# Kernel tuning notes

Measured on AMD Instinct MI355X. Metric: run time of the kernel, lower is better.

The kernel has to match this reference:

```python
import jax, jax.numpy as jnp
import numpy as np

N_NODES = 10000
N_EDGES = 640000
HIDDEN = 128
OUT = 10

def setup_inputs() -> dict:
    key = jax.random.key(0)
    k1, k2, k3, k4 = jax.random.split(key, 4)
    x = jax.random.normal(k1, (N_NODES, HIDDEN), dtype=jnp.float32)
    edge_index = jax.random.randint(k2, (2, N_EDGES), 0, N_NODES, dtype=jnp.int64)
    # ClassifierMLP2 params: Linear(2*hidden -> hidden) -> ReLU -> Linear(hidden -> out)
    W1 = jax.random.normal(k3, (2 * HIDDEN, HIDDEN), dtype=jnp.float32) / np.sqrt(2 * HIDDEN)
    b1 = jnp.zeros((HIDDEN,), dtype=jnp.float32)
    W2 = jax.random.normal(k4, (HIDDEN, OUT), dtype=jnp.float32) / np.sqrt(HIDDEN)
    b2 = jnp.zeros((OUT,), dtype=jnp.float32)
    return {"x": x, "edge_index": edge_index, "W1": W1, "b1": b1, "W2": W2, "b2": b2}

def reference(x, edge_index, W1, b1, W2, b2):
    # mix_node_features(..., node_feat_mixing='cat'): gather src/dst node
    # embeddings per edge and concatenate along feature dim -> [E, 2*H]
    src, dst = edge_index[0], edge_index[1]
    edges_x = jnp.concatenate([x[src], x[dst]], axis=-1)  # [E, 2H]
    # ClassifierMLP2 (dropout inactive at inference)
    h = jax.nn.relu(edges_x @ W1 + b1)                    # [E, H]
    return h @ W2 + b2                                    # [E, OUT]
```

## Files before the change

kernel.cpp:

```cpp
#include <hip/hip_runtime.h>


typedef _Float16 f16;
typedef _Float16 f16x8 __attribute__((ext_vector_type(8)));
typedef float    f32x4 __attribute__((ext_vector_type(4)));

#define HID  128
#define TWOH 256
#define OUTD 10

__global__ __launch_bounds__(256) void prep_weights(
    const float* __restrict__ W1,
    const float* __restrict__ W2,
    f16* __restrict__ W1P,
    f16* __restrict__ W2P)
{
    const int slot = blockIdx.x * 256 + threadIdx.x;
    if (slot < 4096) {
        const int lane = slot & 63, i = slot >> 6;
        const int r = lane & 15, g = lane >> 4;
        const int wv = i >> 4, ct = (i >> 2) & 3, st = i & 3;
        const int c = wv * 64 + ct * 16 + r;
        f16x8 v;
#pragma unroll
        for (int j = 0; j < 8; ++j) {
            const int k = st * 32 + g * 8 + j;
            const float w = (c < HID) ? W1[k * HID + c]
                                      : W1[(HID + k) * HID + (c - HID)];
            v[j] = (f16)w;
        }
        *(f16x8*)(W1P + (long)slot * 8) = v;
    } else if (slot < 4096 + 256) {
        const int s2 = slot - 4096;
        const int lane = s2 & 63, st = s2 >> 6;
        const int r = lane & 15, g = lane >> 4;
        f16x8 v;
#pragma unroll
        for (int j = 0; j < 8; ++j)
            v[j] = (r < OUTD) ? (f16)W2[(st * 32 + g * 8 + j) * OUTD + r] : (f16)0.f;
        *(f16x8*)(W2P + (long)s2 * 8) = v;
    }
}

__global__ __launch_bounds__(256, 3) void node_AB(
    const float* __restrict__ x,
    const f16* __restrict__ W1P,
    const float* __restrict__ b1,
    f16* __restrict__ AB,
    int n_nodes)
{
    const int t = threadIdx.x;
    const int lane = t & 63;
    const int r = lane & 15, g = lane >> 4;
    const int wv = t >> 6;
    const int n0 = blockIdx.x * 16;

    const int xrow = (n0 + r < n_nodes) ? (n0 + r) : (n_nodes - 1);
    float4 xl[4][2];
#pragma unroll
    for (int st = 0; st < 4; ++st) {
        const float* xp = x + (long)xrow * HID + st * 32 + g * 8;
        xl[st][0] = *(const float4*)xp;
        xl[st][1] = *(const float4*)(xp + 4);
    }

    f16x8 w1f[4][4];
    float bias[4];
#pragma unroll
    for (int ct = 0; ct < 4; ++ct) {
        const int c = wv * 64 + ct * 16 + r;
        bias[ct] = (c < HID) ? b1[c] : 0.f;
#pragma unroll
        for (int st = 0; st < 4; ++st)
            w1f[ct][st] = *(const f16x8*)(W1P + ((long)((wv * 16 + ct * 4 + st)) * 64 + lane) * 8);
    }

    f32x4 acc[4] = {{0,0,0,0},{0,0,0,0},{0,0,0,0},{0,0,0,0}};
#pragma unroll
    for (int st = 0; st < 4; ++st) {
        f16x8 a;
        a[0] = (f16)xl[st][0].x; a[1] = (f16)xl[st][0].y;
        a[2] = (f16)xl[st][0].z; a[3] = (f16)xl[st][0].w;
        a[4] = (f16)xl[st][1].x; a[5] = (f16)xl[st][1].y;
        a[6] = (f16)xl[st][1].z; a[7] = (f16)xl[st][1].w;
#pragma unroll
        for (int ct = 0; ct < 4; ++ct)
            acc[ct] = __builtin_amdgcn_mfma_f32_16x16x32_f16(a, w1f[ct][st], acc[ct], 0, 0, 0);
    }

#pragma unroll
    for (int ct = 0; ct < 4; ++ct) {
        const int c = wv * 64 + ct * 16 + r;
#pragma unroll
        for (int q = 0; q < 4; ++q) {
            const int node = n0 + g * 4 + q;
            if (node < n_nodes)
                AB[(long)node * TWOH + c] = (f16)(acc[ct][q] + bias[ct]);
        }
    }
}

__global__ __launch_bounds__(256, 3) void edge_mlp(
    const f16* __restrict__ AB,
    const int* __restrict__ ei,
    const f16* __restrict__ W2P,
    const float* __restrict__ b2,
    float* __restrict__ out,
    int n_edges)
{
    const int t = threadIdx.x;
    const int lane = t & 63;
    const int r = lane & 15, g = lane >> 4;
    const int wv = t >> 6;

    f16x8 w2f[4];
#pragma unroll
    for (int st = 0; st < 4; ++st)
        w2f[st] = *(const f16x8*)(W2P + ((long)st * 64 + lane) * 8);
    const int rc = (r < OUTD) ? r : 0;
    const float bj = b2[rc];

    const f16x8* __restrict__ ABv = (const f16x8*)AB;
    const long eb = (long)blockIdx.x * 512 + wv * 128;

    int sn[8], dn[8];
#pragma unroll
    for (int it = 0; it < 8; ++it) {
        const long e = eb + it * 16 + r;
        const long ec = (e < n_edges) ? e : (n_edges - 1);
        sn[it] = ei[ec];
        dn[it] = ei[(long)n_edges + ec];
    }

    const f16x8 zt = {0, 0, 0, 0, 0, 0, 0, 0};

#define GATHER(Pa, Pc, IT)                                                  \
    f16x8 Pa[4], Pc[4];                                                     \
    {                                                                       \
        const long ab_ = (long)sn[IT] * 32, bb_ = (long)dn[IT] * 32;        \
        _Pragma("unroll")                                                   \
        for (int st = 0; st < 4; ++st) {                                    \
            Pa[st] = ABv[ab_ + st * 4 + g];                                 \
            Pc[st] = ABv[bb_ + 16 + st * 4 + g];                            \
        }                                                                   \
    }

#define COMPSTORE(Pa, Pc, IT)                                               \
    {                                                                       \
        f32x4 acc = {0, 0, 0, 0};                                           \
        _Pragma("unroll")                                                   \
        for (int st = 0; st < 4; ++st) {                                    \
            const f16x8 s = __builtin_elementwise_max(Pa[st] + Pc[st], zt); \
            acc = __builtin_amdgcn_mfma_f32_16x16x32_f16(s, w2f[st], acc, 0, 0, 0); \
        }                                                                   \
        if (r < OUTD) {                                                     \
            _Pragma("unroll")                                               \
            for (int q = 0; q < 4; ++q) {                                   \
                const long ee = eb + IT * 16 + g * 4 + q;                   \
                if (ee < n_edges) out[ee * OUTD + r] = acc[q] + bj;         \
            }                                                               \
        }                                                                   \
    }

    GATHER(a0, c0, 0)
    GATHER(a1, c1, 1)
    GATHER(a2, c2, 2)
    __builtin_amdgcn_sched_barrier(0);
    COMPSTORE(a0, c0, 0)
    GATHER(a3, c3, 3)
    __builtin_amdgcn_sched_barrier(0);
    COMPSTORE(a1, c1, 1)
    GATHER(a4, c4, 4)
    __builtin_amdgcn_sched_barrier(0);
    COMPSTORE(a2, c2, 2)
    GATHER(a5, c5, 5)
    __builtin_amdgcn_sched_barrier(0);
    COMPSTORE(a3, c3, 3)
    GATHER(a6, c6, 6)
    __builtin_amdgcn_sched_barrier(0);
    COMPSTORE(a4, c4, 4)
    GATHER(a7, c7, 7)
    __builtin_amdgcn_sched_barrier(0);
    COMPSTORE(a5, c5, 5)
    COMPSTORE(a6, c6, 6)
    COMPSTORE(a7, c7, 7)

#undef GATHER
#undef COMPSTORE
}

extern "C" void kernel_launch(void* const* d_in, const int* in_sizes, int n_in,
                              void* d_out, int out_size, void* d_ws, size_t ws_size,
                              hipStream_t stream) {
    const float* x  = (const float*)d_in[0];
    const int*   ei = (const int*)d_in[1];
    const float* W1 = (const float*)d_in[2];
    const float* b1 = (const float*)d_in[3];
    const float* W2 = (const float*)d_in[4];
    const float* b2 = (const float*)d_in[5];
    float* out = (float*)d_out;

    const int n_nodes = in_sizes[0] / HID;
    const int n_edges = in_sizes[1] / 2;

    f16* AB  = (f16*)d_ws;
    f16* W1P = AB + (long)n_nodes * TWOH;
    f16* W2P = W1P + 4096 * 8;

    prep_weights<<<17, 256, 0, stream>>>(W1, W2, W1P, W2P);

    node_AB<<<(n_nodes + 15) / 16, 256, 0, stream>>>(x, W1P, b1, AB, n_nodes);

    edge_mlp<<<(n_edges + 511) / 512, 256, 0, stream>>>(AB, ei, W2P, b2, out, n_edges);
}
```

Measured before the change: 61.78 us.

## Hand-schedule edge gathers with inline asm loads and LDS-staged coalesced stores

Replaces compiler-generated gathers in edge_mlp with inline-asm global_load_dwordx4 using immediate offsets, and explicit s_waitcnt vmcnt counts to keep three edge tiles of loads in flight. Output for each 16-edge tile is staged through shared memory so 40 lanes write contiguous dwordx4 stores instead of scattered scalar stores. A scalar fallback path handles partial tiles. This adds asm fragility: the waitcnt counts must match the vector memory ops actually issued, including the interleaved stores.

Measured after the change: 60.35 us. 1.02x faster.

```diff
diff --git a/kernel.cpp b/kernel.cpp
--- a/kernel.cpp
+++ b/kernel.cpp
@@ -108,6 +108,7 @@
     float* __restrict__ out,
     int n_edges)
 {
+    __shared__ float stage[4][160];
     const int t = threadIdx.x;
     const int lane = t & 63;
     const int r = lane & 15, g = lane >> 4;
@@ -117,10 +118,8 @@
 #pragma unroll
     for (int st = 0; st < 4; ++st)
         w2f[st] = *(const f16x8*)(W2P + ((long)st * 64 + lane) * 8);
-    const int rc = (r < OUTD) ? r : 0;
-    const float bj = b2[rc];
-
-    const f16x8* __restrict__ ABv = (const f16x8*)AB;
+    const float bj = b2[(r < OUTD) ? r : 0];
+
     const long eb = (long)blockIdx.x * 512 + wv * 128;
 
     int sn[8], dn[8];
@@ -134,59 +133,96 @@
 
     const f16x8 zt = {0, 0, 0, 0, 0, 0, 0, 0};
 
-#define GATHER(Pa, Pc, IT)                                                  \
-    f16x8 Pa[4], Pc[4];                                                     \
-    {                                                                       \
-        const long ab_ = (long)sn[IT] * 32, bb_ = (long)dn[IT] * 32;        \
-        _Pragma("unroll")                                                   \
-        for (int st = 0; st < 4; ++st) {                                    \
-            Pa[st] = ABv[ab_ + st * 4 + g];                                 \
-            Pc[st] = ABv[bb_ + 16 + st * 4 + g];                            \
-        }                                                                   \
-    }
-
-#define COMPSTORE(Pa, Pc, IT)                                               \
-    {                                                                       \
-        f32x4 acc = {0, 0, 0, 0};                                           \
-        _Pragma("unroll")                                                   \
-        for (int st = 0; st < 4; ++st) {                                    \
-            const f16x8 s = __builtin_elementwise_max(Pa[st] + Pc[st], zt); \
-            acc = __builtin_amdgcn_mfma_f32_16x16x32_f16(s, w2f[st], acc, 0, 0, 0); \
-        }                                                                   \
-        if (r < OUTD) {                                                     \
-            _Pragma("unroll")                                               \
-            for (int q = 0; q < 4; ++q) {                                   \
-                const long ee = eb + IT * 16 + g * 4 + q;                   \
-                if (ee < n_edges) out[ee * OUTD + r] = acc[q] + bj;         \
-            }                                                               \
-        }                                                                   \
-    }
-
-    GATHER(a0, c0, 0)
-    GATHER(a1, c1, 1)
-    GATHER(a2, c2, 2)
+    if (eb + 128 <= n_edges) {
+        asm volatile("" ::
+            "v"(w2f[0]), "v"(w2f[1]), "v"(w2f[2]), "v"(w2f[3]), "v"(bj),
+            "v"(sn[0]), "v"(sn[1]), "v"(sn[2]), "v"(sn[3]),
+            "v"(sn[4]), "v"(sn[5]), "v"(sn[6]), "v"(sn[7]),
+            "v"(dn[0]), "v"(dn[1]), "v"(dn[2]), "v"(dn[3]),
+            "v"(dn[4]), "v"(dn[5]), "v"(dn[6]), "v"(dn[7]));
+
+#define DECL(IT) f16x8 pa##IT##0, pa##IT##1, pa##IT##2, pa##IT##3, \
+                       pc##IT##0, pc##IT##1, pc##IT##2, pc##IT##3;
+        DECL(0) DECL(1) DECL(2) DECL(3) DECL(4) DECL(5) DECL(6) DECL(7)
+
+#define ISSUE(IT) { \
+    const f16* _pa = AB + ((long)sn[IT] * TWOH + g * 8); \
+    const f16* _pb = AB + ((long)dn[IT] * TWOH + HID + g * 8); \
+    asm volatile("global_load_dwordx4 %0, %1, off"            : "=v"(pa##IT##0) : "v"(_pa)); \
+    asm volatile("global_load_dwordx4 %0, %1, off offset:64"  : "=v"(pa##IT##1) : "v"(_pa)); \
+    asm volatile("global_load_dwordx4 %0, %1, off offset:128" : "=v"(pa##IT##2) : "v"(_pa)); \
+    asm volatile("global_load_dwordx4 %0, %1, off offset:192" : "=v"(pa##IT##3) : "v"(_pa)); \
+    asm volatile("global_load_dwordx4 %0, %1, off"            : "=v"(pc##IT##0) : "v"(_pb)); \
+    asm volatile("global_load_dwordx4 %0, %1, off offset:64"  : "=v"(pc##IT##1) : "v"(_pb)); \
+    asm volatile("global_load_dwordx4 %0, %1, off offset:128" : "=v"(pc##IT##2) : "v"(_pb)); \
+    asm volatile("global_load_dwordx4 %0, %1, off offset:192" : "=v"(pc##IT##3) : "v"(_pb)); \
+}
+
+#define WAITN(IT, NSTR) \
+    asm volatile("s_waitcnt vmcnt(" NSTR ")" \
+        : "+v"(pa##IT##0), "+v"(pa##IT##1), "+v"(pa##IT##2), "+v"(pa##IT##3), \
+          "+v"(pc##IT##0), "+v"(pc##IT##1), "+v"(pc##IT##2), "+v"(pc##IT##3)); \
     __builtin_amdgcn_sched_barrier(0);
-    COMPSTORE(a0, c0, 0)
-    GATHER(a3, c3, 3)
-    __builtin_amdgcn_sched_barrier(0);
-    COMPSTORE(a1, c1, 1)
-    GATHER(a4, c4, 4)
-    __builtin_amdgcn_sched_barrier(0);
-    COMPSTORE(a2, c2, 2)
-    GATHER(a5, c5, 5)
-    __builtin_amdgcn_sched_barrier(0);
-    COMPSTORE(a3, c3, 3)
-    GATHER(a6, c6, 6)
-    __builtin_amdgcn_sched_barrier(0);
-    COMPSTORE(a4, c4, 4)
-    GATHER(a7, c7, 7)
-    __builtin_amdgcn_sched_barrier(0);
-    COMPSTORE(a5, c5, 5)
-    COMPSTORE(a6, c6, 6)
-    COMPSTORE(a7, c7, 7)
-
-#undef GATHER
-#undef COMPSTORE
+
+#define COMPUTE(IT) { \
+    f32x4 acc = {0, 0, 0, 0}; \
+    f16x8 s; \
+    s = __builtin_elementwise_max(pa##IT##0 + pc##IT##0, zt); \
+    acc = __builtin_amdgcn_mfma_f32_16x16x32_f16(s, w2f[0], acc, 0, 0, 0); \
+    s = __builtin_elementwise_max(pa##IT##1 + pc##IT##1, zt); \
+    acc = __builtin_amdgcn_mfma_f32_16x16x32_f16(s, w2f[1], acc, 0, 0, 0); \
+    s = __builtin_elementwise_max(pa##IT##2 + pc##IT##2, zt); \
+    acc = __builtin_amdgcn_mfma_f32_16x16x32_f16(s, w2f[2], acc, 0, 0, 0); \
+    s = __builtin_elementwise_max(pa##IT##3 + pc##IT##3, zt); \
+    acc = __builtin_amdgcn_mfma_f32_16x16x32_f16(s, w2f[3], acc, 0, 0, 0); \
+    if (r < OUTD) { \
+        _Pragma("unroll") \
+        for (int q = 0; q < 4; ++q) \
+            stage[wv][(g * 4 + q) * OUTD + r] = acc[q] + bj; \
+    } \
+    __builtin_amdgcn_wave_barrier(); \
+    if (lane < 40) { \
+        const f32x4 vv = *(const f32x4*)&stage[wv][lane * 4]; \
+        float* po = out + (eb + IT * 16) * OUTD + lane * 4; \
+        asm volatile("global_store_dwordx4 %0, %1, off" :: "v"(po), "v"(vv) : "memory"); \
+    } \
+    __builtin_amdgcn_wave_barrier(); \
+}
+
+        ISSUE(0) ISSUE(1) ISSUE(2)
+        WAITN(0, "16") COMPUTE(0) ISSUE(3)
+        WAITN(1, "17") COMPUTE(1) ISSUE(4)
+        WAITN(2, "18") COMPUTE(2) ISSUE(5)
+        WAITN(3, "18") COMPUTE(3) ISSUE(6)
+        WAITN(4, "18") COMPUTE(4) ISSUE(7)
+        WAITN(5, "18") COMPUTE(5)
+        WAITN(6, "10") COMPUTE(6)
+        WAITN(7, "2")  COMPUTE(7)
+        asm volatile("s_waitcnt vmcnt(0)");
+#undef DECL
+#undef ISSUE
+#undef WAITN
+#undef COMPUTE
+    } else {
+#pragma unroll
+        for (int it = 0; it < 8; ++it) {
+            f32x4 acc = {0, 0, 0, 0};
+#pragma unroll
+            for (int st = 0; st < 4; ++st) {
+                const f16x8 a = *(const f16x8*)(AB + ((long)sn[it] * TWOH + st * 32 + g * 8));
+                const f16x8 c = *(const f16x8*)(AB + ((long)dn[it] * TWOH + HID + st * 32 + g * 8));
+                const f16x8 s = __builtin_elementwise_max(a + c, zt);
+                acc = __builtin_amdgcn_mfma_f32_16x16x32_f16(s, w2f[st], acc, 0, 0, 0);
+            }
+            if (r < OUTD) {
+#pragma unroll
+                for (int q = 0; q < 4; ++q) {
+                    const long ee = eb + it * 16 + g * 4 + q;
+                    if (ee < n_edges) out[ee * OUTD + r] = acc[q] + bj;
+                }
+            }
+        }
+    }
 }
 
 extern "C" void kernel_launch(void* const* d_in, const int* in_sizes, int n_in,
```
